# Performance work log

Measured on AMD Instinct MI355X. Metric: run time of the kernel, lower is better.

Reference implementation:

```python
import jax, jax.numpy as jnp
import numpy as np

TAU = 0.07
EPS = 1e-12  # torch F.normalize eps


def _conv2d(x, w, b, stride):
    # x: (N, Cin, H, W), w: (Cout, Cin, kh, kw)
    y = jax.lax.conv_general_dilated(
        x, w, window_strides=(stride, stride), padding='SAME',
        dimension_numbers=('NCHW', 'OIHW', 'NCHW'))
    return y + b[None, :, None, None]


def _encoder(x, conv1_w, conv1_b, conv2_w, conv2_b, lin_w, lin_b):
    # x: (BTN, 1, H, W) -> (BTN, emb_dim)
    h = jax.nn.relu(_conv2d(x, conv1_w, conv1_b, 2))   # (BTN, 32, H/2, W/2)
    h = jax.nn.relu(_conv2d(h, conv2_w, conv2_b, 2))   # (BTN, 64, H/4, W/4)
    h = h.mean(axis=(2, 3))                            # global avg pool -> (BTN, 64)
    return h @ lin_w + lin_b                           # (BTN, emb_dim)


def setup_inputs() -> dict:
    key = jax.random.key(0)
    ks = jax.random.split(key, 4)
    B, T, N, H, W = 8, 10, 128, 32, 32
    seq = jax.random.normal(ks[0], (B, T, N, H, W), dtype=jnp.float32)
    conv1_w = jax.random.normal(ks[1], (32, 1, 3, 3), dtype=jnp.float32) * (1.0 / 3.0)
    conv1_b = jnp.zeros((32,), jnp.float32)
    conv2_w = jax.random.normal(ks[2], (64, 32, 3, 3), dtype=jnp.float32) * (1.0 / np.sqrt(32 * 9))
    conv2_b = jnp.zeros((64,), jnp.float32)
    lin_w = jax.random.normal(ks[3], (64, 128), dtype=jnp.float32) * (1.0 / 8.0)
    lin_b = jnp.zeros((128,), jnp.float32)
    return {"seq": seq, "conv1_w": conv1_w, "conv1_b": conv1_b,
            "conv2_w": conv2_w, "conv2_b": conv2_b, "lin_w": lin_w, "lin_b": lin_b}


def reference(seq, conv1_w, conv1_b, conv2_w, conv2_b, lin_w, lin_b):
    B, T, N, H, W = seq.shape
    x = seq.reshape(-1, 1, H, W)
    emb = _encoder(x, conv1_w, conv1_b, conv2_w, conv2_b, lin_w, lin_b)
    emb = emb.reshape(B, T, N, -1)
    # L2 normalize along feature dim (torch F.normalize semantics)
    nrm = jnp.sqrt(jnp.sum(emb * emb, axis=-1, keepdims=True))
    emb = emb / jnp.maximum(nrm, EPS)
    # pairwise affinities between consecutive frames: (B, T-1, N, N)
    A = jnp.einsum('btnc,btmc->btnm', emb[:, :-1], emb[:, 1:]) / TAU
    # forward + time-reversed (transposed) affinities: (B, 2(T-1), N, N)
    AA = jnp.concatenate([A, jnp.swapaxes(jnp.flip(A, axis=1), -1, -2)], axis=1)
    S = jax.nn.softmax(AA, axis=-1)  # row-stochastic transition matrices
    I = jnp.eye(N, dtype=seq.dtype)
    loss = jnp.zeros((), seq.dtype)
    for k in range(1, T - 1):
        S_this = jnp.concatenate([S[:, :k], S[:, -k:]], axis=1)  # (B, 2k, N, N)
        At = jnp.broadcast_to(I, (B, N, N))
        for t in range(1, 2 * k):  # note: index 0 unused, matching original
            At = jnp.matmul(S_this[:, t], At)
        # cross_entropy(input=At (B,C=N,d=N), target=eye) with soft targets:
        # mean over (B, d) of -log_softmax(At, class_dim=1)[b, j, j]
        logp = jax.nn.log_softmax(At, axis=1)
        loss = loss - jnp.mean(jnp.diagonal(logp, axis1=1, axis2=2))
    return (loss / N, A)
```

## Files before the change

kernel.cpp:

```cpp
#include <hip/hip_runtime.h>
#include <math.h>

typedef _Float16 f16;
typedef f16 f16x8 __attribute__((ext_vector_type(8)));
typedef f16 f16x4 __attribute__((ext_vector_type(4)));
typedef float f32x4 __attribute__((ext_vector_type(4)));

__global__ __launch_bounds__(256) void k_repack(const float* __restrict__ w2,
                                                const float* __restrict__ lw,
                                                f16* __restrict__ w2p,
                                                float* __restrict__ lwT,
                                                float* __restrict__ lossAcc) {
  int i = blockIdx.x * 256 + threadIdx.x;
  if (i == 0) lossAcc[0] = 0.f;
  if (i < 18432) {
    const int ic = i & 31, oc = (i >> 5) & 63, tap = i >> 11;
    const float w = w2[oc * 288 + ic * 9 + tap];
    const f16 wh = (f16)w;
    w2p[i] = wh;
    w2p[18432 + i] = (f16)(w - (float)wh);
  }
  if (i < 8192) lwT[i] = lw[(i & 63) * 128 + (i >> 6)];
}

__global__ __launch_bounds__(256, 4) void k_encoder(
    const float* __restrict__ seq,
    const float* __restrict__ w1, const float* __restrict__ b1,
    const f16* __restrict__ w2p, const float* __restrict__ b2,
    const float* __restrict__ lwT, const float* __restrict__ lb,
    f16* __restrict__ emb16)
{
  __shared__ float s_in[33 * 33];
  __shared__ __align__(16) f16 s_h1[289 * 40];
  __shared__ __align__(16) float s_pool[64];
  __shared__ float s_part[2];
  const int t = threadIdx.x;
  const int lane = t & 63, wv = t >> 6;
  const int wvs = __builtin_amdgcn_readfirstlane(wv);

  const float* x = seq + (size_t)blockIdx.x * 1024;
  for (int i = t; i < 1024; i += 256)
    s_in[(i >> 5) * 33 + (i & 31)] = x[i];
  if (t < 33) s_in[32 * 33 + t] = 0.f;
  if (t < 32) s_in[t * 33 + 32] = 0.f;
  if (t < 132) {
    const int zi = t >> 2, ch = t & 3;
    const int row = (zi < 16) ? zi * 17 + 16 : 272 + (zi - 16);
    *(f32x4*)&s_h1[row * 40 + ch * 8] = f32x4{0.f, 0.f, 0.f, 0.f};
  }
  float cw[8][9], cb[8];
  {
    const float* wp = w1 + wvs * 72;
#pragma unroll
    for (int j = 0; j < 8; ++j) {
#pragma unroll
      for (int q = 0; q < 9; ++q)
        cw[j][q] = __uint_as_float(__builtin_amdgcn_readfirstlane(__float_as_uint(wp[j * 9 + q])));
      cb[j] = __uint_as_float(__builtin_amdgcn_readfirstlane(__float_as_uint(b1[wvs * 8 + j])));
    }
  }
  __syncthreads();
#pragma unroll
  for (int i = 0; i < 4; ++i) {
    const int pos = lane + 64 * i, oy = pos >> 4, ox = pos & 15;
    float p[9];
#pragma unroll
    for (int dy = 0; dy < 3; ++dy)
#pragma unroll
      for (int dx = 0; dx < 3; ++dx)
        p[dy * 3 + dx] = s_in[(2 * oy + dy) * 33 + 2 * ox + dx];
    f16x8 o;
#pragma unroll
    for (int j = 0; j < 8; ++j) {
      float a = cb[j];
#pragma unroll
      for (int q = 0; q < 9; ++q) a = fmaf(p[q], cw[j][q], a);
      o[j] = (f16)fmaxf(a, 0.f);
    }
    *(f16x8*)&s_h1[(oy * 17 + ox) * 40 + 8 * wv] = o;
  }
  f16x8 bh[9], bl[9];
  float bias2;
  {
    const int oc = wv * 16 + (lane & 15);
    const int o8 = ((lane >> 4) & 3) * 8;
#pragma unroll
    for (int tap = 0; tap < 9; ++tap) {
      bh[tap] = *(const f16x8*)(w2p + ((tap * 64 + oc) * 32 + o8));
      bl[tap] = *(const f16x8*)(w2p + 18432 + ((tap * 64 + oc) * 32 + o8));
    }
    bias2 = b2[wv * 16 + (lane & 15)];
  }
  __syncthreads();
  {
    const int lr = lane & 15, o8 = (lane >> 4) & 3;
    f32x4 acc[4];
#pragma unroll
    for (int m = 0; m < 4; ++m) acc[m] = f32x4{bias2, bias2, bias2, bias2};
#pragma unroll
    for (int m = 0; m < 4; ++m) {
      const int opos = m * 16 + lr, oy = opos >> 3, ox = opos & 7;
      const int baddr = (34 * oy + 2 * ox) * 40 + o8 * 8;
#pragma unroll
      for (int dy = 0; dy < 3; ++dy)
#pragma unroll
        for (int dx = 0; dx < 3; ++dx) {
          const int tap = dy * 3 + dx;
          f16x8 afr = *(const f16x8*)&s_h1[baddr + (dy * 17 + dx) * 40];
          acc[m] = __builtin_amdgcn_mfma_f32_16x16x32_f16(afr, bh[tap], acc[m], 0, 0, 0);
          acc[m] = __builtin_amdgcn_mfma_f32_16x16x32_f16(afr, bl[tap], acc[m], 0, 0, 0);
        }
    }
    float s = 0.f;
#pragma unroll
    for (int m = 0; m < 4; ++m)
#pragma unroll
      for (int v = 0; v < 4; ++v) s += fmaxf(acc[m][v], 0.f);
    s += __shfl_xor(s, 16, 64);
    s += __shfl_xor(s, 32, 64);
    if (lane < 16) s_pool[wv * 16 + lane] = s * (1.f / 64.f);
  }
  __syncthreads();
  float val = 0.f;
  if (t < 128) {
    val = lb[t];
    const float* lr = lwT + t * 64;
#pragma unroll
    for (int c4 = 0; c4 < 16; ++c4) {
      const f32x4 wv4 = *(const f32x4*)(lr + c4 * 4);
      const f32x4 pv = *(const f32x4*)&s_pool[c4 * 4];
      val = fmaf(pv[0], wv4[0], val);
      val = fmaf(pv[1], wv4[1], val);
      val = fmaf(pv[2], wv4[2], val);
      val = fmaf(pv[3], wv4[3], val);
    }
  }
  float sq = val * val;
#pragma unroll
  for (int off = 1; off < 64; off <<= 1) sq += __shfl_xor(sq, off, 64);
  if (t < 128 && (t & 63) == 0) s_part[t >> 6] = sq;
  __syncthreads();
  if (t < 128) {
    const float nrm = sqrtf(s_part[0] + s_part[1]);
    emb16[(size_t)blockIdx.x * 128 + t] = (f16)(val / fmaxf(nrm, 1e-12f));
  }
}

__global__ __launch_bounds__(256) void k_affinity(const f16* __restrict__ emb16,
                                                  float* __restrict__ Aout)
{
  __shared__ __align__(16) f16 sL[16384];
  __shared__ __align__(16) f16 sR[16384];
  const int bid = blockIdx.x, b = bid / 9, tt = bid % 9;
  const int t = threadIdx.x, lane = t & 63, w = t >> 6;
  const int lr = lane & 15, lg = lane >> 4;
  const f16* Ea = emb16 + (size_t)(b * 10 + tt) * 16384;
  const f16* Eb = Ea + 16384;
#pragma unroll
  for (int j = 0; j < 8; ++j) {
    const int ck = j * 256 + t, row = ck >> 4, c16 = ck & 15;
    const int off = ((row << 8) + (c16 << 4)) ^ ((row & 7) << 4);
    *(f16x8*)((char*)sL + off) = *(const f16x8*)(Ea + ck * 8);
    *(f16x8*)((char*)sR + off) = *(const f16x8*)(Eb + ck * 8);
  }
  __syncthreads();
  f32x4 acc[2][8] = {};
#pragma unroll
  for (int kt = 0; kt < 4; ++kt) {
    int row = w * 32 + lr;
    int byt = ((row << 8) + kt * 64 + (lg << 4)) ^ ((row & 7) << 4);
    const f16x8 a0 = *(const f16x8*)((char*)sL + byt);
    row += 16;
    byt = ((row << 8) + kt * 64 + (lg << 4)) ^ ((row & 7) << 4);
    const f16x8 a1 = *(const f16x8*)((char*)sL + byt);
#pragma unroll
    for (int nt = 0; nt < 8; ++nt) {
      const int rb = nt * 16 + lr;
      const int bb = ((rb << 8) + kt * 64 + (lg << 4)) ^ ((rb & 7) << 4);
      const f16x8 bv = *(const f16x8*)((char*)sR + bb);
      acc[0][nt] = __builtin_amdgcn_mfma_f32_16x16x32_f16(a0, bv, acc[0][nt], 0, 0, 0);
      acc[1][nt] = __builtin_amdgcn_mfma_f32_16x16x32_f16(a1, bv, acc[1][nt], 0, 0, 0);
    }
  }
  float* Og = Aout + (size_t)bid * 16384;
#pragma unroll
  for (int mt = 0; mt < 2; ++mt)
#pragma unroll
    for (int nt = 0; nt < 8; ++nt)
#pragma unroll
      for (int v = 0; v < 4; ++v) {
        const int r = w * 32 + mt * 16 + lg * 4 + v, c = nt * 16 + lr;
        Og[r * 128 + c] = acc[mt][nt][v] * (1.f / 0.07f);
      }
}

__global__ __launch_bounds__(128) void k_softmax(const float* __restrict__ A,
                                                 f16* __restrict__ Srow, f16* __restrict__ ST,
                                                 float* __restrict__ loss)
{
  __shared__ __align__(16) f16 sT[128 * 136];
  __shared__ float s_m[128], s_d[128], s_m2[128], s_d2[128];
  __shared__ float s_red[2];
  const int bid = blockIdx.x, b = bid / 9, tt = bid % 9;
  const float* Ag = A + (size_t)bid * 16384;
  const int t = threadIdx.x;
  float m1 = -1e30f, m2 = -1e30f, s1 = 0.f, s2 = 0.f;
#pragma unroll 4
  for (int r = 0; r < 128; ++r) {
    m2 = fmaxf(m2, Ag[r * 128 + t]);
    m1 = fmaxf(m1, Ag[t * 128 + r]);
  }
#pragma unroll 4
  for (int r = 0; r < 128; ++r) {
    s2 += expf(Ag[r * 128 + t] - m2);
    s1 += expf(Ag[t * 128 + r] - m1);
  }
  s_m[t] = m1; s_d[t] = 1.f / s1;
  s_m2[t] = m2; s_d2[t] = 1.f / s2;
  __syncthreads();
  f16* Sfg = Srow + (size_t)(b * 18 + tt) * 16384;
  f16* SfTg = ST + (size_t)(b * 18 + tt) * 16384;
  f16* Sbg = Srow + (size_t)(b * 18 + 17 - tt) * 16384;
  f16* SbTg = ST + (size_t)(b * 18 + 17 - tt) * 16384;
  for (int r = 0; r < 128; ++r) {
    const float v1 = expf(Ag[r * 128 + t] - s_m[r]) * s_d[r];
    Sfg[r * 128 + t] = (f16)v1;
    sT[t * 136 + r] = (f16)v1;
  }
  __syncthreads();
#pragma unroll
  for (int j = 0; j < 16; ++j) {
    const int ck = j * 128 + t, c = ck >> 4, c16 = ck & 15;
    *(f16x8*)(SfTg + ck * 8) = *(const f16x8*)&sT[c * 136 + c16 * 8];
  }
  __syncthreads();
  float s3 = 0.f, d3 = 0.f;
  for (int r = 0; r < 128; ++r) {
    const float v2 = expf(Ag[t * 128 + r] - s_m2[r]) * s_d2[r];
    Sbg[r * 128 + t] = (f16)v2;
    sT[t * 136 + r] = (f16)v2;
    if (tt == 0) {
      s3 += expf(v2);
      if (r == t) d3 = v2;
    }
  }
  __syncthreads();
#pragma unroll
  for (int j = 0; j < 16; ++j) {
    const int ck = j * 128 + t, c = ck >> 4, c16 = ck & 15;
    *(f16x8*)(SbTg + ck * 8) = *(const f16x8*)&sT[c * 136 + c16 * 8];
  }
  if (tt == 0) {
    float lp = d3 - logf(s3);
#pragma unroll
    for (int off = 1; off < 64; off <<= 1) lp += __shfl_xor(lp, off, 64);
    if ((t & 63) == 0) s_red[t >> 6] = lp;
    __syncthreads();
    if (t == 0) atomicAdd(loss, s_red[0] + s_red[1]);
  }
}

__global__ __launch_bounds__(256) void k_chain(
    int k,
    const f16* __restrict__ Srow, const f16* __restrict__ ST,
    f16* __restrict__ Pcur, const f16* __restrict__ Pprev,
    f16* __restrict__ FTcur, const f16* __restrict__ FTprev,
    float* __restrict__ loss)
{
  __shared__ __align__(16) f16 sL[16384];
  __shared__ __align__(16) f16 sRt[16384];
  const int role = blockIdx.x >> 3, b = blockIdx.x & 7;
  const int t = threadIdx.x, lane = t & 63, w = t >> 6;
  const int lr = lane & 15, lg = lane >> 4;

  const f16 *L, *Rt;
  if (role == 0) {
    if (k > 8) return;
    L = (k == 2) ? (Srow + (size_t)(b * 18 + 17) * 16384) : (Pprev + (size_t)b * 16384);
    Rt = ST + (size_t)(b * 18 + (18 - k)) * 16384;
  } else if (role == 1) {
    if (k < 3 || k > 8) return;
    L = Srow + (size_t)(b * 18 + (k - 1)) * 16384;
    Rt = (k == 3) ? (ST + (size_t)(b * 18 + 1) * 16384) : (FTprev + (size_t)b * 16384);
  } else {
    if (k < 3) return;
    L = Pprev + (size_t)b * 16384;
    Rt = (k == 3) ? (ST + (size_t)(b * 18 + 1) * 16384) : (FTprev + (size_t)b * 16384);
  }
#pragma unroll
  for (int j = 0; j < 8; ++j) {
    const int ck = j * 256 + t, row = ck >> 4, c16 = ck & 15;
    const int off = ((row << 8) + (c16 << 4)) ^ ((row & 7) << 4);
    *(f16x8*)((char*)sL + off) = *(const f16x8*)(L + ck * 8);
    *(f16x8*)((char*)sRt + off) = *(const f16x8*)(Rt + ck * 8);
  }
  __syncthreads();
  f32x4 acc[2][8] = {};
#pragma unroll
  for (int kt = 0; kt < 4; ++kt) {
    int row = w * 32 + lr;
    int byt = ((row << 8) + kt * 64 + (lg << 4)) ^ ((row & 7) << 4);
    const f16x8 a0 = *(const f16x8*)((char*)sL + byt);
    row += 16;
    byt = ((row << 8) + kt * 64 + (lg << 4)) ^ ((row & 7) << 4);
    const f16x8 a1 = *(const f16x8*)((char*)sL + byt);
#pragma unroll
    for (int nt = 0; nt < 8; ++nt) {
      const int rb = nt * 16 + lr;
      const int bb = ((rb << 8) + kt * 64 + (lg << 4)) ^ ((rb & 7) << 4);
      const f16x8 bv = *(const f16x8*)((char*)sRt + bb);
      acc[0][nt] = __builtin_amdgcn_mfma_f32_16x16x32_f16(a0, bv, acc[0][nt], 0, 0, 0);
      acc[1][nt] = __builtin_amdgcn_mfma_f32_16x16x32_f16(a1, bv, acc[1][nt], 0, 0, 0);
    }
  }
  if (role == 0) {
    f16* P = Pcur + (size_t)b * 16384;
#pragma unroll
    for (int mt = 0; mt < 2; ++mt)
#pragma unroll
      for (int nt = 0; nt < 8; ++nt)
#pragma unroll
        for (int v = 0; v < 4; ++v)
          P[(w * 32 + mt * 16 + lg * 4 + v) * 128 + nt * 16 + lr] = (f16)acc[mt][nt][v];
  } else if (role == 1) {
    f16* FT = FTcur + (size_t)b * 16384;
#pragma unroll
    for (int mt = 0; mt < 2; ++mt)
#pragma unroll
      for (int nt = 0; nt < 8; ++nt) {
        f16x4 pk;
#pragma unroll
        for (int v = 0; v < 4; ++v) pk[v] = (f16)acc[mt][nt][v];
        *(f16x4*)(FT + (size_t)(nt * 16 + lr) * 128 + w * 32 + mt * 16 + lg * 4) = pk;
      }
  } else {
    __syncthreads();
    float* redm = (float*)sL;
    float* redM = redm + 512;
    float* reds = redM + 128;
    float* redL = reds + 512;
    float* redW = redL + 128;
#pragma unroll
    for (int nt = 0; nt < 8; ++nt) {
      float pm = -1e30f;
#pragma unroll
      for (int mt = 0; mt < 2; ++mt)
#pragma unroll
        for (int v = 0; v < 4; ++v) pm = fmaxf(pm, acc[mt][nt][v]);
      pm = fmaxf(pm, __shfl_xor(pm, 16, 64));
      pm = fmaxf(pm, __shfl_xor(pm, 32, 64));
      if (lg == 0) redm[(nt * 16 + lr) * 4 + w] = pm;
    }
    __syncthreads();
    if (t < 128) redM[t] = fmaxf(fmaxf(redm[t * 4], redm[t * 4 + 1]),
                                 fmaxf(redm[t * 4 + 2], redm[t * 4 + 3]));
    __syncthreads();
#pragma unroll
    for (int nt = 0; nt < 8; ++nt) {
      const float mc = redM[nt * 16 + lr];
      float ps = 0.f;
#pragma unroll
      for (int mt = 0; mt < 2; ++mt)
#pragma unroll
        for (int v = 0; v < 4; ++v) ps += expf(acc[mt][nt][v] - mc);
      ps += __shfl_xor(ps, 16, 64);
      ps += __shfl_xor(ps, 32, 64);
      if (lg == 0) reds[(nt * 16 + lr) * 4 + w] = ps;
    }
    __syncthreads();
    if (t < 128) redL[t] = logf(reds[t * 4] + reds[t * 4 + 1] + reds[t * 4 + 2] + reds[t * 4 + 3]);
    __syncthreads();
    float contrib = 0.f;
#pragma unroll
    for (int mt = 0; mt < 2; ++mt)
#pragma unroll
      for (int nt = 0; nt < 8; ++nt)
#pragma unroll
        for (int v = 0; v < 4; ++v) {
          const int r = w * 32 + mt * 16 + lg * 4 + v, c = nt * 16 + lr;
          if (r == c) contrib += acc[mt][nt][v] - redM[c] - redL[c];
        }
#pragma unroll
    for (int off = 1; off < 64; off <<= 1) contrib += __shfl_xor(contrib, off, 64);
    if (lane == 0) redW[w] = contrib;
    __syncthreads();
    if (t == 0) atomicAdd(loss, redW[0] + redW[1] + redW[2] + redW[3]);
  }
}

__global__ void k_final(const float* __restrict__ acc, float* __restrict__ out) {
  out[0] = -acc[0] * (1.f / 131072.f);
}

extern "C" void kernel_launch(void* const* d_in, const int* in_sizes, int n_in,
                              void* d_out, int out_size, void* d_ws, size_t ws_size,
                              hipStream_t stream) {
  const float* seq = (const float*)d_in[0];
  const float* w1  = (const float*)d_in[1];
  const float* b1  = (const float*)d_in[2];
  const float* w2  = (const float*)d_in[3];
  const float* b2  = (const float*)d_in[4];
  const float* lw  = (const float*)d_in[5];
  const float* lb  = (const float*)d_in[6];
  float* out = (float*)d_out;

  f16* emb16 = (f16*)d_ws;
  f16* Srow  = emb16 + 1310720;
  f16* ST    = Srow + 2359296;
  f16* Pb    = ST + 2359296;
  f16* FTb   = Pb + 262144;
  f16* w2p   = FTb + 262144;
  float* lwT = (float*)(w2p + 36864);
  float* lossAcc = lwT + 8192;

  float* Aout = out + 1;

  k_repack<<<72, 256, 0, stream>>>(w2, lw, w2p, lwT, lossAcc);
  k_encoder<<<10240, 256, 0, stream>>>(seq, w1, b1, w2p, b2, lwT, lb, emb16);
  k_affinity<<<72, 256, 0, stream>>>(emb16, Aout);
  k_softmax<<<72, 128, 0, stream>>>(Aout, Srow, ST, lossAcc);
  for (int k = 2; k <= 9; ++k) {
    const int cur = k & 1, prev = cur ^ 1;
    k_chain<<<24, 256, 0, stream>>>(k, Srow, ST,
        Pb + cur * 131072, Pb + prev * 131072,
        FTb + cur * 131072, FTb + prev * 131072,
        lossAcc);
  }
  k_final<<<1, 1, 0, stream>>>(lossAcc, out);
}
```

Before: 294.1 us.

## Run conv1 on MFMA with split-f16 weights and fuse affinity with softmax

The first convolution moves from per-thread scalar FMAs to MFMA instructions. The 9 taps are packed into a 32-wide K dimension, with the f16 high part of each weight in one half and its f16 residual in the other, to keep accuracy. The affinity and softmax kernels become one kernel that computes row and column softmax straight from the MFMA accumulators, so the A matrix is no longer read back from global memory and one launch disappears. It also writes only the S slices the chain uses. The inputs are rounded to f16 for conv1, which adds precision risk, and the fused kernel uses more shared memory.

```diff
diff --git a/kernel.cpp b/kernel.cpp
--- a/kernel.cpp
+++ b/kernel.cpp
@@ -7,11 +7,13 @@
 typedef float f32x4 __attribute__((ext_vector_type(4)));
 
 __global__ __launch_bounds__(256) void k_repack(const float* __restrict__ w2,
+                                                const float* __restrict__ w1,
                                                 const float* __restrict__ lw,
                                                 f16* __restrict__ w2p,
+                                                f16* __restrict__ w1p,
                                                 float* __restrict__ lwT,
                                                 float* __restrict__ lossAcc) {
-  int i = blockIdx.x * 256 + threadIdx.x;
+  const int i = blockIdx.x * 256 + threadIdx.x;
   if (i == 0) lossAcc[0] = 0.f;
   if (i < 18432) {
     const int ic = i & 31, oc = (i >> 5) & 63, tap = i >> 11;
@@ -20,12 +22,22 @@
     w2p[i] = wh;
     w2p[18432 + i] = (f16)(w - (float)wh);
   }
+  if (i < 1024) {
+    const int oc = i >> 5, k = i & 31;
+    f16 r = (f16)0.f;
+    if (k < 9) r = (f16)w1[oc * 9 + k];
+    else if (k >= 16 && k < 25) {
+      const float w = w1[oc * 9 + (k - 16)];
+      r = (f16)(w - (float)((f16)w));
+    }
+    w1p[i] = r;
+  }
   if (i < 8192) lwT[i] = lw[(i & 63) * 128 + (i >> 6)];
 }
 
 __global__ __launch_bounds__(256, 4) void k_encoder(
     const float* __restrict__ seq,
-    const float* __restrict__ w1, const float* __restrict__ b1,
+    const f16* __restrict__ w1p, const float* __restrict__ b1,
     const f16* __restrict__ w2p, const float* __restrict__ b2,
     const float* __restrict__ lwT, const float* __restrict__ lb,
     f16* __restrict__ emb16)
@@ -34,9 +46,8 @@
   __shared__ __align__(16) f16 s_h1[289 * 40];
   __shared__ __align__(16) float s_pool[64];
   __shared__ float s_part[2];
-  const int t = threadIdx.x;
-  const int lane = t & 63, wv = t >> 6;
-  const int wvs = __builtin_amdgcn_readfirstlane(wv);
+  const int t = threadIdx.x, lane = t & 63, wv = t >> 6;
+  const int lr = lane & 15, lg = lane >> 4;
 
   const float* x = seq + (size_t)blockIdx.x * 1024;
   for (int i = t; i < 1024; i += 256)
@@ -48,65 +59,74 @@
     const int row = (zi < 16) ? zi * 17 + 16 : 272 + (zi - 16);
     *(f32x4*)&s_h1[row * 40 + ch * 8] = f32x4{0.f, 0.f, 0.f, 0.f};
   }
-  float cw[8][9], cb[8];
+  f16x8 w1f[2];
+  float b1v[2];
+#pragma unroll
+  for (int n = 0; n < 2; ++n) {
+    w1f[n] = *(const f16x8*)(w1p + (n * 16 + lr) * 32 + lg * 8);
+    b1v[n] = b1[n * 16 + lr];
+  }
+  __syncthreads();
+
   {
-    const float* wp = w1 + wvs * 72;
-#pragma unroll
-    for (int j = 0; j < 8; ++j) {
-#pragma unroll
-      for (int q = 0; q < 9; ++q)
-        cw[j][q] = __uint_as_float(__builtin_amdgcn_readfirstlane(__float_as_uint(wp[j * 9 + q])));
-      cb[j] = __uint_as_float(__builtin_amdgcn_readfirstlane(__float_as_uint(b1[wvs * 8 + j])));
-    }
-  }
-  __syncthreads();
-#pragma unroll
-  for (int i = 0; i < 4; ++i) {
-    const int pos = lane + 64 * i, oy = pos >> 4, ox = pos & 15;
-    float p[9];
-#pragma unroll
-    for (int dy = 0; dy < 3; ++dy)
-#pragma unroll
-      for (int dx = 0; dx < 3; ++dx)
-        p[dy * 3 + dx] = s_in[(2 * oy + dy) * 33 + 2 * ox + dx];
-    f16x8 o;
-#pragma unroll
-    for (int j = 0; j < 8; ++j) {
-      float a = cb[j];
-#pragma unroll
-      for (int q = 0; q < 9; ++q) a = fmaf(p[q], cw[j][q], a);
-      o[j] = (f16)fmaxf(a, 0.f);
-    }
-    *(f16x8*)&s_h1[(oy * 17 + ox) * 40 + 8 * wv] = o;
+    const bool odd = lg & 1;
+    f32x4 a1[4][2];
+#pragma unroll
+    for (int m = 0; m < 4; ++m) {
+      const int oy = wv * 4 + m;
+      const int base = 66 * oy + 2 * lr;
+      f16x8 af;
+      af[0] = (f16)s_in[base + (odd ? 68 : 0)];
+      { const float v = s_in[base + 1];  af[1] = odd ? (f16)0.f : (f16)v; }
+      { const float v = s_in[base + 2];  af[2] = odd ? (f16)0.f : (f16)v; }
+      { const float v = s_in[base + 33]; af[3] = odd ? (f16)0.f : (f16)v; }
+      { const float v = s_in[base + 34]; af[4] = odd ? (f16)0.f : (f16)v; }
+      { const float v = s_in[base + 35]; af[5] = odd ? (f16)0.f : (f16)v; }
+      { const float v = s_in[base + 66]; af[6] = odd ? (f16)0.f : (f16)v; }
+      { const float v = s_in[base + 67]; af[7] = odd ? (f16)0.f : (f16)v; }
+#pragma unroll
+      for (int n = 0; n < 2; ++n) {
+        const f32x4 c0 = f32x4{b1v[n], b1v[n], b1v[n], b1v[n]};
+        a1[m][n] = __builtin_amdgcn_mfma_f32_16x16x32_f16(af, w1f[n], c0, 0, 0, 0);
+      }
+    }
+#pragma unroll
+    for (int m = 0; m < 4; ++m) {
+      const int oy = wv * 4 + m;
+#pragma unroll
+      for (int n = 0; n < 2; ++n)
+#pragma unroll
+        for (int v = 0; v < 4; ++v)
+          s_h1[(oy * 17 + lg * 4 + v) * 40 + n * 16 + lr] = (f16)fmaxf(a1[m][n][v], 0.f);
+    }
   }
   f16x8 bh[9], bl[9];
   float bias2;
   {
-    const int oc = wv * 16 + (lane & 15);
-    const int o8 = ((lane >> 4) & 3) * 8;
+    const int oc = wv * 16 + lr;
 #pragma unroll
     for (int tap = 0; tap < 9; ++tap) {
-      bh[tap] = *(const f16x8*)(w2p + ((tap * 64 + oc) * 32 + o8));
-      bl[tap] = *(const f16x8*)(w2p + 18432 + ((tap * 64 + oc) * 32 + o8));
-    }
-    bias2 = b2[wv * 16 + (lane & 15)];
-  }
-  __syncthreads();
+      bh[tap] = *(const f16x8*)(w2p + ((tap * 64 + oc) * 32 + lg * 8));
+      bl[tap] = *(const f16x8*)(w2p + 18432 + ((tap * 64 + oc) * 32 + lg * 8));
+    }
+    bias2 = b2[oc];
+  }
+  __syncthreads();
+
   {
-    const int lr = lane & 15, o8 = (lane >> 4) & 3;
     f32x4 acc[4];
 #pragma unroll
     for (int m = 0; m < 4; ++m) acc[m] = f32x4{bias2, bias2, bias2, bias2};
 #pragma unroll
     for (int m = 0; m < 4; ++m) {
       const int opos = m * 16 + lr, oy = opos >> 3, ox = opos & 7;
-      const int baddr = (34 * oy + 2 * ox) * 40 + o8 * 8;
+      const int baddr = (34 * oy + 2 * ox) * 40 + lg * 8;
 #pragma unroll
       for (int dy = 0; dy < 3; ++dy)
 #pragma unroll
         for (int dx = 0; dx < 3; ++dx) {
           const int tap = dy * 3 + dx;
-          f16x8 afr = *(const f16x8*)&s_h1[baddr + (dy * 17 + dx) * 40];
+          const f16x8 afr = *(const f16x8*)&s_h1[baddr + (dy * 17 + dx) * 40];
           acc[m] = __builtin_amdgcn_mfma_f32_16x16x32_f16(afr, bh[tap], acc[m], 0, 0, 0);
           acc[m] = __builtin_amdgcn_mfma_f32_16x16x32_f16(afr, bl[tap], acc[m], 0, 0, 0);
         }
@@ -124,10 +144,10 @@
   float val = 0.f;
   if (t < 128) {
     val = lb[t];
-    const float* lr = lwT + t * 64;
+    const float* lrow = lwT + t * 64;
 #pragma unroll
     for (int c4 = 0; c4 < 16; ++c4) {
-      const f32x4 wv4 = *(const f32x4*)(lr + c4 * 4);
+      const f32x4 wv4 = *(const f32x4*)(lrow + c4 * 4);
       const f32x4 pv = *(const f32x4*)&s_pool[c4 * 4];
       val = fmaf(pv[0], wv4[0], val);
       val = fmaf(pv[1], wv4[1], val);
@@ -146,11 +166,16 @@
   }
 }
 
-__global__ __launch_bounds__(256) void k_affinity(const f16* __restrict__ emb16,
-                                                  float* __restrict__ Aout)
+__global__ __launch_bounds__(256) void k_affsm(
+    const f16* __restrict__ emb16, float* __restrict__ Aout,
+    f16* __restrict__ Srow, f16* __restrict__ ST, float* __restrict__ loss)
 {
   __shared__ __align__(16) f16 sL[16384];
   __shared__ __align__(16) f16 sR[16384];
+  __shared__ __align__(16) f16 sT[128 * 136];
+  __shared__ float s_cm[128], s_cd[128];
+  __shared__ float s_red4[512];
+  __shared__ float s_lred[4];
   const int bid = blockIdx.x, b = bid / 9, tt = bid % 9;
   const int t = threadIdx.x, lane = t & 63, w = t >> 6;
   const int lr = lane & 15, lg = lane >> 4;
@@ -182,81 +207,129 @@
       acc[1][nt] = __builtin_amdgcn_mfma_f32_16x16x32_f16(a1, bv, acc[1][nt], 0, 0, 0);
     }
   }
+#pragma unroll
+  for (int mt = 0; mt < 2; ++mt)
+#pragma unroll
+    for (int nt = 0; nt < 8; ++nt)
+#pragma unroll
+      for (int v = 0; v < 4; ++v) acc[mt][nt][v] *= (1.f / 0.07f);
+
   float* Og = Aout + (size_t)bid * 16384;
 #pragma unroll
   for (int mt = 0; mt < 2; ++mt)
 #pragma unroll
     for (int nt = 0; nt < 8; ++nt)
 #pragma unroll
-      for (int v = 0; v < 4; ++v) {
-        const int r = w * 32 + mt * 16 + lg * 4 + v, c = nt * 16 + lr;
-        Og[r * 128 + c] = acc[mt][nt][v] * (1.f / 0.07f);
+      for (int v = 0; v < 4; ++v)
+        Og[(w * 32 + mt * 16 + lg * 4 + v) * 128 + nt * 16 + lr] = acc[mt][nt][v];
+
+  float rm[2][4], rd[2][4];
+#pragma unroll
+  for (int mt = 0; mt < 2; ++mt)
+#pragma unroll
+    for (int v = 0; v < 4; ++v) {
+      float m = -1e30f;
+#pragma unroll
+      for (int nt = 0; nt < 8; ++nt) m = fmaxf(m, acc[mt][nt][v]);
+      m = fmaxf(m, __shfl_xor(m, 1, 64));
+      m = fmaxf(m, __shfl_xor(m, 2, 64));
+      m = fmaxf(m, __shfl_xor(m, 4, 64));
+      m = fmaxf(m, __shfl_xor(m, 8, 64));
+      float s = 0.f;
+#pragma unroll
+      for (int nt = 0; nt < 8; ++nt) s += expf(acc[mt][nt][v] - m);
+      s += __shfl_xor(s, 1, 64);
+      s += __shfl_xor(s, 2, 64);
+      s += __shfl_xor(s, 4, 64);
+      s += __shfl_xor(s, 8, 64);
+      rm[mt][v] = m;
+      rd[mt][v] = 1.f / s;
+    }
+#pragma unroll
+  for (int nt = 0; nt < 8; ++nt) {
+    float m = -1e30f;
+#pragma unroll
+    for (int mt = 0; mt < 2; ++mt)
+#pragma unroll
+      for (int v = 0; v < 4; ++v) m = fmaxf(m, acc[mt][nt][v]);
+    m = fmaxf(m, __shfl_xor(m, 16, 64));
+    m = fmaxf(m, __shfl_xor(m, 32, 64));
+    if (lg == 0) s_red4[(nt * 16 + lr) * 4 + w] = m;
+  }
+  __syncthreads();
+  if (t < 128) s_cm[t] = fmaxf(fmaxf(s_red4[t * 4], s_red4[t * 4 + 1]),
+                               fmaxf(s_red4[t * 4 + 2], s_red4[t * 4 + 3]));
+  __syncthreads();
+#pragma unroll
+  for (int nt = 0; nt < 8; ++nt) {
+    const float mc = s_cm[nt * 16 + lr];
+    float s = 0.f;
+#pragma unroll
+    for (int mt = 0; mt < 2; ++mt)
+#pragma unroll
+      for (int v = 0; v < 4; ++v) s += expf(acc[mt][nt][v] - mc);
+    s += __shfl_xor(s, 16, 64);
+    s += __shfl_xor(s, 32, 64);
+    if (lg == 0) s_red4[(nt * 16 + lr) * 4 + w] = s;
+  }
+  __syncthreads();
+  if (t < 128) s_cd[t] = 1.f / (s_red4[t * 4] + s_red4[t * 4 + 1] +
+                                s_red4[t * 4 + 2] + s_red4[t * 4 + 3]);
+  __syncthreads();
+
+  const bool wantSfD = (tt >= 2 && tt <= 7);
+  const bool wantSfT = (tt == 1);
+  const bool wantSbD = (tt >= 1 && tt <= 7);
+  const bool wantSbT = (tt == 0);
+  f16* SfD = Srow + (size_t)(b * 18 + tt) * 16384;
+  f16* SbD = ST + (size_t)(b * 18 + 17 - tt) * 16384;
+
+  float contrib = 0.f;
+#pragma unroll
+  for (int mt = 0; mt < 2; ++mt)
+#pragma unroll
+    for (int v = 0; v < 4; ++v) {
+      const int r = w * 32 + mt * 16 + lg * 4 + v;
+      float qsum = 0.f, dval = 0.f;
+#pragma unroll
+      for (int nt = 0; nt < 8; ++nt) {
+        const int c = nt * 16 + lr;
+        const float a = acc[mt][nt][v];
+        const float sf = expf(a - rm[mt][v]) * rd[mt][v];
+        const float sb = expf(a - s_cm[c]) * s_cd[c];
+        if (wantSfD) SfD[r * 128 + c] = (f16)sf;
+        if (wantSbD) SbD[r * 128 + c] = (f16)sb;
+        if (wantSfT) sT[c * 136 + r] = (f16)sf;
+        if (wantSbT) {
+          sT[c * 136 + r] = (f16)sb;
+          qsum += expf(sb);
+          if (nt == (w * 2 + mt)) dval = sb;
+        }
       }
-}
-
-__global__ __launch_bounds__(128) void k_softmax(const float* __restrict__ A,
-                                                 f16* __restrict__ Srow, f16* __restrict__ ST,
-                                                 float* __restrict__ loss)
-{
-  __shared__ __align__(16) f16 sT[128 * 136];
-  __shared__ float s_m[128], s_d[128], s_m2[128], s_d2[128];
-  __shared__ float s_red[2];
-  const int bid = blockIdx.x, b = bid / 9, tt = bid % 9;
-  const float* Ag = A + (size_t)bid * 16384;
-  const int t = threadIdx.x;
-  float m1 = -1e30f, m2 = -1e30f, s1 = 0.f, s2 = 0.f;
-#pragma unroll 4
-  for (int r = 0; r < 128; ++r) {
-    m2 = fmaxf(m2, Ag[r * 128 + t]);
-    m1 = fmaxf(m1, Ag[t * 128 + r]);
-  }
-#pragma unroll 4
-  for (int r = 0; r < 128; ++r) {
-    s2 += expf(Ag[r * 128 + t] - m2);
-    s1 += expf(Ag[t * 128 + r] - m1);
-  }
-  s_m[t] = m1; s_d[t] = 1.f / s1;
-  s_m2[t] = m2; s_d2[t] = 1.f / s2;
-  __syncthreads();
-  f16* Sfg = Srow + (size_t)(b * 18 + tt) * 16384;
-  f16* SfTg = ST + (size_t)(b * 18 + tt) * 16384;
-  f16* Sbg = Srow + (size_t)(b * 18 + 17 - tt) * 16384;
-  f16* SbTg = ST + (size_t)(b * 18 + 17 - tt) * 16384;
-  for (int r = 0; r < 128; ++r) {
-    const float v1 = expf(Ag[r * 128 + t] - s_m[r]) * s_d[r];
-    Sfg[r * 128 + t] = (f16)v1;
-    sT[t * 136 + r] = (f16)v1;
-  }
-  __syncthreads();
-#pragma unroll
-  for (int j = 0; j < 16; ++j) {
-    const int ck = j * 128 + t, c = ck >> 4, c16 = ck & 15;
-    *(f16x8*)(SfTg + ck * 8) = *(const f16x8*)&sT[c * 136 + c16 * 8];
-  }
-  __syncthreads();
-  float s3 = 0.f, d3 = 0.f;
-  for (int r = 0; r < 128; ++r) {
-    const float v2 = expf(Ag[t * 128 + r] - s_m2[r]) * s_d2[r];
-    Sbg[r * 128 + t] = (f16)v2;
-    sT[t * 136 + r] = (f16)v2;
-    if (tt == 0) {
-      s3 += expf(v2);
-      if (r == t) d3 = v2;
-    }
-  }
-  __syncthreads();
-#pragma unroll
-  for (int j = 0; j < 16; ++j) {
-    const int ck = j * 128 + t, c = ck >> 4, c16 = ck & 15;
-    *(f16x8*)(SbTg + ck * 8) = *(const f16x8*)&sT[c * 136 + c16 * 8];
-  }
-  if (tt == 0) {
-    float lp = d3 - logf(s3);
-#pragma unroll
-    for (int off = 1; off < 64; off <<= 1) lp += __shfl_xor(lp, off, 64);
-    if ((t & 63) == 0) s_red[t >> 6] = lp;
-    __syncthreads();
-    if (t == 0) atomicAdd(loss, s_red[0] + s_red[1]);
+      if (wantSbT) {
+        qsum += __shfl_xor(qsum, 1, 64);
+        qsum += __shfl_xor(qsum, 2, 64);
+        qsum += __shfl_xor(qsum, 4, 64);
+        qsum += __shfl_xor(qsum, 8, 64);
+        if (lr == lg * 4 + v) contrib += dval - logf(qsum);
+      }
+    }
+  if (wantSfT || wantSbT) {
+    __syncthreads();
+    f16* dst = wantSfT ? (ST + (size_t)(b * 18 + 1) * 16384)
+                       : (Srow + (size_t)(b * 18 + 17) * 16384);
+#pragma unroll
+    for (int j = 0; j < 8; ++j) {
+      const int e = (j * 256 + t) * 8;
+      *(f16x8*)(dst + e) = *(const f16x8*)&sT[(e >> 7) * 136 + (e & 127)];
+    }
+  }
+  if (wantSbT) {
+#pragma unroll
+    for (int off = 1; off < 64; off <<= 1) contrib += __shfl_xor(contrib, off, 64);
+    if (lane == 0) s_lred[w] = contrib;
+    __syncthreads();
+    if (t == 0) atomicAdd(loss, s_lred[0] + s_lred[1] + s_lred[2] + s_lred[3]);
   }
 }
 
@@ -368,7 +441,8 @@
       if (lg == 0) reds[(nt * 16 + lr) * 4 + w] = ps;
     }
     __syncthreads();
-    if (t < 128) redL[t] = logf(reds[t * 4] + reds[t * 4 + 1] + reds[t * 4 + 2] + reds[t * 4 + 3]);
+    if (t < 128) redL[t] = logf(reds[t * 4] + reds[t * 4 + 1] +
+                                reds[t * 4 + 2] + reds[t * 4 + 3]);
     __syncthreads();
     float contrib = 0.f;
 #pragma unroll
@@ -410,15 +484,15 @@
   f16* Pb    = ST + 2359296;
   f16* FTb   = Pb + 262144;
   f16* w2p   = FTb + 262144;
-  float* lwT = (float*)(w2p + 36864);
+  f16* w1p   = w2p + 36864;
+  float* lwT = (float*)(w1p + 1024);
   float* lossAcc = lwT + 8192;
 
   float* Aout = out + 1;
 
-  k_repack<<<72, 256, 0, stream>>>(w2, lw, w2p, lwT, lossAcc);
-  k_encoder<<<10240, 256, 0, stream>>>(seq, w1, b1, w2p, b2, lwT, lb, emb16);
-  k_affinity<<<72, 256, 0, stream>>>(emb16, Aout);
-  k_softmax<<<72, 128, 0, stream>>>(Aout, Srow, ST, lossAcc);
+  k_repack<<<72, 256, 0, stream>>>(w2, w1, lw, w2p, w1p, lwT, lossAcc);
+  k_encoder<<<10240, 256, 0, stream>>>(seq, w1p, b1, w2p, b2, lwT, lb, emb16);
+  k_affsm<<<72, 256, 0, stream>>>(emb16, Aout, Srow, ST, lossAcc);
   for (int k = 2; k <= 9; ++k) {
     const int cur = k & 1, prev = cur ^ 1;
     k_chain<<<24, 256, 0, stream>>>(k, Srow, ST,
```

Result: faster. 276.5 us (-6.0%).
